# Kernel tuning notes

Hardware: AMD Instinct MI355X
Metric: run time of the kernel (lower is better)

## Reference

```python
import jax, jax.numpy as jnp
import numpy as np

C = 64           # channels
CPG = 8          # channel_per_group
G = C // CPG     # offset groups = 8
K = 27           # 3x3x3 taps
N, D, H, W = 2, 8, 56, 56


def conv3d(x, w, b=None):
    y = jax.lax.conv_general_dilated(
        x, w, window_strides=(1, 1, 1), padding=[(1, 1)] * 3,
        dimension_numbers=('NCDHW', 'OIDHW', 'NCDHW'))
    if b is not None:
        y = y + b.reshape(1, -1, 1, 1, 1)
    return y


def deform_conv3d(x, off, w, groups):
    # x: [N,C,D,H,W]; off: [N, G*3*27, D,H,W]; w: [O,C,3,3,3]
    n, cin, d, h, wd = x.shape
    cpg = cin // groups
    p = d * h * wd
    off = off.reshape(n, groups, K, 3, d, h, wd)
    # kernel tap displacements in (kd,kh,kw) order, each in {-1,0,1}
    r = jnp.arange(3, dtype=x.dtype) - 1.0
    taps = jnp.stack(jnp.meshgrid(r, r, r, indexing='ij'), axis=-1).reshape(K, 3)
    gd = jnp.arange(d, dtype=x.dtype)[:, None, None]
    gh = jnp.arange(h, dtype=x.dtype)[None, :, None]
    gw = jnp.arange(wd, dtype=x.dtype)[None, None, :]
    # sampling positions [N,G,K,D,H,W]
    pd = gd + taps[:, 0][:, None, None, None] + off[:, :, :, 0]
    ph = gh + taps[:, 1][:, None, None, None] + off[:, :, :, 1]
    pw = gw + taps[:, 2][:, None, None, None] + off[:, :, :, 2]
    d0 = jnp.floor(pd); h0 = jnp.floor(ph); w0 = jnp.floor(pw)
    fd, fh, fw = pd - d0, ph - h0, pw - w0
    d0 = d0.astype(jnp.int32); h0 = h0.astype(jnp.int32); w0 = w0.astype(jnp.int32)
    xflat = x.reshape(n, groups, cpg, p)[:, :, None]  # [N,G,1,Cpg,P]
    acc = jnp.zeros((n, groups, K, cpg, p), x.dtype)
    for cd in (0, 1):
        for ch in (0, 1):
            for cw in (0, 1):
                idd, idh, idw = d0 + cd, h0 + ch, w0 + cw
                wgt = ((fd if cd else 1.0 - fd)
                       * (fh if ch else 1.0 - fh)
                       * (fw if cw else 1.0 - fw))
                valid = ((idd >= 0) & (idd < d) & (idh >= 0) & (idh < h)
                         & (idw >= 0) & (idw < wd)).astype(x.dtype)
                lin = ((jnp.clip(idd, 0, d - 1) * h + jnp.clip(idh, 0, h - 1)) * wd
                       + jnp.clip(idw, 0, wd - 1))
                g = jnp.take_along_axis(xflat, lin.reshape(n, groups, K, 1, p), axis=-1)
                acc = acc + g * (wgt * valid).reshape(n, groups, K, 1, p)
    # [N,G,K,Cpg,P] -> [N,K,C,P]
    vals = acc.transpose(0, 2, 1, 3, 4).reshape(n, K, cin, p)
    out = jnp.einsum('oik,nkip->nop', w.reshape(w.shape[0], cin, K), vals)
    return out.reshape(n, -1, d, h, wd)


def batchnorm(x, gamma, beta, eps=1e-5):
    m = x.mean((0, 2, 3, 4), keepdims=True)
    v = x.var((0, 2, 3, 4), keepdims=True)
    return (gamma.reshape(1, -1, 1, 1, 1) * (x - m) * jax.lax.rsqrt(v + eps)
            + beta.reshape(1, -1, 1, 1, 1))


def setup_inputs() -> dict:
    key = jax.random.key(0)
    ks = jax.random.split(key, 4)
    fan = C * K
    x = jax.random.normal(ks[0], (N, C, D, H, W), jnp.float32)
    w_off = jax.random.normal(ks[1], (G * 3 * K, C, 3, 3, 3), jnp.float32) * 0.01
    b_off = jnp.zeros((G * 3 * K,), jnp.float32)
    w1 = jax.random.normal(ks[2], (C, C, 3, 3, 3), jnp.float32) / np.sqrt(fan).astype(np.float32)
    w2 = jax.random.normal(ks[3], (C, C, 3, 3, 3), jnp.float32) / np.sqrt(fan).astype(np.float32)
    return dict(x=x, w_off=w_off, b_off=b_off, w1=w1,
                gamma1=jnp.ones((C,), jnp.float32), beta1=jnp.zeros((C,), jnp.float32),
                w2=w2, b2=jnp.zeros((C,), jnp.float32),
                gamma2=jnp.ones((C,), jnp.float32), beta2=jnp.zeros((C,), jnp.float32))


def reference(x, w_off, b_off, w1, gamma1, beta1, w2, b2, gamma2, beta2):
    residual = x
    off = conv3d(x, w_off, b_off)
    out = deform_conv3d(x, off, w1, G)
    out = jax.nn.relu(batchnorm(out, gamma1, beta1))
    out = conv3d(out, w2, b2)
    out = batchnorm(out, gamma2, beta2) + residual
    return jax.nn.relu(out)
```

## Files before the change

kernel.cpp:

```cpp
#include <hip/hip_runtime.h>
#include <hip/hip_bf16.h>

#define N_ 2
#define C_ 64
#define D_ 8
#define H_ 56
#define W_ 56
#define HW_ (H_*W_)
#define P_ (D_*HW_)
#define G_ 8
#define CPG_ 8
#define K_ 27
#define CO_OFF_ 648
#define MP_ 768
#define KK_ 1728
#define KB_ (KK_*2)

typedef __attribute__((ext_vector_type(8))) short shortx8;
typedef __attribute__((ext_vector_type(4))) float floatx4;
#define AS1 __attribute__((address_space(1)))
#define AS3 __attribute__((address_space(3)))

__device__ inline float b2f(unsigned short u) {
    union { unsigned u; float f; } x; x.u = ((unsigned)u) << 16; return x.f;
}
__device__ inline unsigned short f2b(float f) {
    union { float f; unsigned u; } x; x.f = f;
    unsigned r = (x.u + 0x7fffu + ((x.u >> 16) & 1u)) >> 16;
    return (unsigned short)r;
}
__device__ inline float lof(unsigned u) { union { unsigned u; float f; } x; x.u = u << 16; return x.f; }
__device__ inline float hif(unsigned u) { union { unsigned u; float f; } x; x.u = u & 0xffff0000u; return x.f; }
__device__ inline unsigned cvt_pk_bf16(float a, float b) {
    unsigned r;
    asm("v_cvt_pk_bf16_f32 %0, %1, %2" : "=v"(r) : "v"(a), "v"(b));
    return r;
}


__global__ __launch_bounds__(256) void transpose_xt_kernel(
    const float* __restrict__ x, unsigned short* __restrict__ xt)
{
    __shared__ unsigned short tile[64][65];
    int b  = blockIdx.x;
    int n  = b / (P_/64);
    int p0 = (b % (P_/64))*64;
    int tid = threadIdx.x;
    int j  = tid & 63;
    int c0 = (tid >> 6)*16;
    for (int r = 0; r < 16; ++r)
        tile[c0 + r][j] = f2b(x[((size_t)n*C_ + c0 + r)*P_ + p0 + j]);
    __syncthreads();
    unsigned* dst = (unsigned*)(xt + ((size_t)n*P_ + p0)*C_);
    #pragma unroll
    for (int it = 0; it < 8; ++it) {
        int wi  = it*256 + tid;
        int row = wi >> 5;
        int c   = (wi & 31)*2;
        unsigned lo = tile[c][row], hi = tile[c+1][row];
        dst[(size_t)row*32 + (wi & 31)] = lo | (hi << 16);
    }
}

__global__ __launch_bounds__(256) void permA1k_kernel(
    const float* __restrict__ w, unsigned short* __restrict__ A)
{
    int i = blockIdx.x*256 + threadIdx.x;
    if (i >= MP_*KK_) return;
    int m = i / KK_, r = i % KK_;
    int kk = r / 64, ci = r % 64;
    A[i] = (m < CO_OFF_) ? f2b(w[((size_t)m*C_ + ci)*K_ + kk]) : (unsigned short)0;
}

__global__ __launch_bounds__(256) void perm_w_kernel(
    const float* __restrict__ w, unsigned short* __restrict__ At)
{
    int tid = blockIdx.x*256 + threadIdx.x;
    if (tid >= C_*KK_) return;
    int o  = tid / KK_;
    int r  = tid % KK_;
    int k  = r / 64, i = r % 64;
    At[tid] = f2b(w[((size_t)o*C_ + i)*K_ + k]);
}

__global__ __launch_bounds__(256, 2) void conv_off_fused(
    const unsigned short* __restrict__ A,
    const unsigned short* __restrict__ xt,
    const float* __restrict__ bias,
    unsigned short* __restrict__ off2)
{
    __shared__ __align__(16) short SH[35840];
    int tid = threadIdx.x;
    int w = tid >> 6, lane = tid & 63;
    int lm = lane & 15, lq = lane >> 4;

    if (blockIdx.x < 2*490) {
        short* As0 = SH;
        short* Bs  = SH + 2*16*512;
        int n   = blockIdx.x / 490;
        int bid = blockIdx.x % 490;
        int mt = bid / 98, nt = bid % 98;
        int m0 = mt*128, p0 = nt*256;

        const unsigned short* xtn = xt + (size_t)n*P_*C_;
        unsigned short* out2 = off2 + (size_t)n*216*P_*3;

        const char* Ab0 = (const char*)A + (size_t)(m0 + w*32 + lm)*KB_ + lq*16;
        const char* Ab1 = Ab0 + (size_t)16*KB_;

        int oct = lane & 7;
        int prj[8], dj[8], hj[8], wj[8];
        #pragma unroll
        for (int j = 0; j < 8; ++j) {
            int prow = j*32 + w*8 + (lane >> 3);
            prj[j] = prow;
            int p = p0 + prow;
            dj[j] = p / HW_;
            int hw2 = p % HW_;
            hj[j] = hw2 / W_;
            wj[j] = hw2 % W_;
        }

        auto stageA = [&](int kt, int buf) {
            __builtin_amdgcn_global_load_lds((const AS1 unsigned*)(Ab0 + kt*128),      (AS3 unsigned*)(As0 + buf*8192 + (w*2)*512),     16, 0, 0);
            __builtin_amdgcn_global_load_lds((const AS1 unsigned*)(Ab1 + kt*128),      (AS3 unsigned*)(As0 + buf*8192 + (w*2+1)*512),   16, 0, 0);
            __builtin_amdgcn_global_load_lds((const AS1 unsigned*)(Ab0 + kt*128 + 64), (AS3 unsigned*)(As0 + buf*8192 + (8+w*2)*512),   16, 0, 0);
            __builtin_amdgcn_global_load_lds((const AS1 unsigned*)(Ab1 + kt*128 + 64), (AS3 unsigned*)(As0 + buf*8192 + (8+w*2+1)*512), 16, 0, 0);
        };
        auto loadB = [&](int kt, uint4* B) {
            int kd = kt/9 - 1, kh = (kt/3)%3 - 1, kw = kt%3 - 1;
            int delta = kd*HW_ + kh*W_ + kw;
            #pragma unroll
            for (int j = 0; j < 8; ++j) {
                bool v = ((unsigned)(dj[j]+kd) < (unsigned)D_) &&
                         ((unsigned)(hj[j]+kh) < (unsigned)H_) &&
                         ((unsigned)(wj[j]+kw) < (unsigned)W_);
                uint4 val = {0u,0u,0u,0u};
                if (v) val = *(const uint4*)(xtn + (size_t)(p0 + prj[j] + delta)*C_ + oct*8);
                B[j] = val;
            }
        };

        int mh = w >> 1, nh = w & 1;
        floatx4 acc[4][8];
        #pragma unroll
        for (int i = 0; i < 4; ++i)
            #pragma unroll
            for (int j = 0; j < 8; ++j)
                acc[i][j] = (floatx4){0.f, 0.f, 0.f, 0.f};

        uint4 Bcur[8], Bnext[8];
        #pragma unroll
        for (int j = 0; j < 8; ++j) Bnext[j] = (uint4){0u,0u,0u,0u};
        stageA(0, 0);
        loadB(0, Bcur);

        for (int kt = 0; kt < 27; ++kt) {
            int buf = kt & 1;
            __syncthreads();
            #pragma unroll
            for (int j = 0; j < 8; ++j) {
                int chunk = (oct>>2)*16 + (prj[j]>>4);
                *(uint4*)&Bs[chunk*512 + ((oct&3)*16 + ((prj[j]&15) ^ oct))*8] = Bcur[j];
            }
            __syncthreads();
            if (kt < 26) { stageA(kt+1, buf^1); loadB(kt+1, Bnext); }
            #pragma unroll
            for (int ks = 0; ks < 2; ++ks) {
                int swzB = (lq*16 + (lm ^ (ks*4 + lq)))*8;
                shortx8 a[4];
                #pragma unroll
                for (int i = 0; i < 4; ++i) a[i] = *(const shortx8*)&As0[buf*8192 + (ks*8 + 4*mh + i)*512 + lane*8];
                #pragma unroll
                for (int j = 0; j < 8; ++j) {
                    shortx8 b = *(const shortx8*)&Bs[(ks*16 + 8*nh + j)*512 + swzB];
                    #pragma unroll
                    for (int i = 0; i < 4; ++i)
                        acc[i][j] = __builtin_amdgcn_mfma_f32_16x16x32_bf16(a[i], b, acc[i][j], 0, 0, 0);
                }
            }
            #pragma unroll
            for (int j = 0; j < 8; ++j) Bcur[j] = Bnext[j];
        }

        #pragma unroll
        for (int i = 0; i < 4; ++i) {
            int cob = m0 + (4*mh+i)*16 + lq*4;
            #pragma unroll
            for (int r = 0; r < 4; ++r) {
                int co = cob + r;
                float bv = bias[co];
                int row2 = co / 3, comp = co % 3;
                size_t base = (size_t)row2*P_*3 + comp;
                #pragma unroll
                for (int j = 0; j < 8; ++j) {
                    int col = p0 + (8*nh+j)*16 + lm;
                    out2[base + (size_t)col*3] = f2b(acc[i][j][r] + bv);
                }
            }
        }
    } else {
        short* As = SH;
        short* Bs = SH + 54*512;
        int t  = blockIdx.x - 2*490;
        int n  = t / 196;
        int p0 = (t % 196)*128;

        const unsigned short* xtn = xt + (size_t)n*P_*C_;
        unsigned short* out2 = off2 + (size_t)n*216*P_*3;

        const char* Abase = (const char*)A + (size_t)(640 + lm)*KB_ + lq*16;
        for (int ch = w; ch < 54; ch += 4)
            __builtin_amdgcn_global_load_lds((const AS1 unsigned*)(Abase + ch*64),
                                             (AS3 unsigned*)(As + ch*512), 16, 0, 0);

        int oct = lane & 7;
        int prj[4], dj[4], hj[4], wj[4];
        #pragma unroll
        for (int j = 0; j < 4; ++j) {
            int prow = j*32 + w*8 + (lane >> 3);
            prj[j] = prow;
            int p = p0 + prow;
            dj[j] = p / HW_;
            int hw2 = p % HW_;
            hj[j] = hw2 / W_;
            wj[j] = hw2 % W_;
        }
        auto loadB = [&](int kt, uint4* B) {
            int kd = kt/9 - 1, kh = (kt/3)%3 - 1, kw = kt%3 - 1;
            int delta = kd*HW_ + kh*W_ + kw;
            #pragma unroll
            for (int j = 0; j < 4; ++j) {
                bool v = ((unsigned)(dj[j]+kd) < (unsigned)D_) &&
                         ((unsigned)(hj[j]+kh) < (unsigned)H_) &&
                         ((unsigned)(wj[j]+kw) < (unsigned)W_);
                uint4 val = {0u,0u,0u,0u};
                if (v) val = *(const uint4*)(xtn + (size_t)(p0 + prj[j] + delta)*C_ + oct*8);
                B[j] = val;
            }
        };

        floatx4 acc[2];
        acc[0] = (floatx4){0.f,0.f,0.f,0.f};
        acc[1] = (floatx4){0.f,0.f,0.f,0.f};

        uint4 Bcur[4], Bnext[4];
        #pragma unroll
        for (int j = 0; j < 4; ++j) Bnext[j] = (uint4){0u,0u,0u,0u};
        loadB(0, Bcur);

        for (int kt = 0; kt < 27; ++kt) {
            __syncthreads();
            #pragma unroll
            for (int j = 0; j < 4; ++j) {
                int chunk = (oct>>2)*8 + (prj[j]>>4);
                *(uint4*)&Bs[chunk*512 + ((oct&3)*16 + ((prj[j]&15) ^ oct))*8] = Bcur[j];
            }
            __syncthreads();
            if (kt < 26) loadB(kt+1, Bnext);
            #pragma unroll
            for (int ks = 0; ks < 2; ++ks) {
                int swzB = (lq*16 + (lm ^ (ks*4 + lq)))*8;
                shortx8 a = *(const shortx8*)&As[(kt*2 + ks)*512 + lane*8];
                #pragma unroll
                for (int j = 0; j < 2; ++j) {
                    shortx8 b = *(const shortx8*)&Bs[(ks*8 + w*2 + j)*512 + swzB];
                    acc[j] = __builtin_amdgcn_mfma_f32_16x16x32_bf16(a, b, acc[j], 0, 0, 0);
                }
            }
            #pragma unroll
            for (int j = 0; j < 4; ++j) Bcur[j] = Bnext[j];
        }

        #pragma unroll
        for (int j = 0; j < 2; ++j) {
            #pragma unroll
            for (int r = 0; r < 4; ++r) {
                int co = 640 + lq*4 + r;
                if (co < CO_OFF_) {
                    int col = p0 + w*32 + j*16 + lm;
                    out2[((size_t)(co/3)*P_ + col)*3 + (co%3)] = f2b(acc[j][r] + bias[co]);
                }
            }
        }
    }
}

__global__ __launch_bounds__(256) void deform_fused(
    const unsigned short* __restrict__ xt,
    const unsigned short* __restrict__ off2,
    const unsigned short* __restrict__ A,
    unsigned short* __restrict__ y1t)
{
    __shared__ __align__(16) short SH[12288];
    int tid = threadIdx.x;
    int w = tid >> 6, lane = tid & 63;
    int n  = blockIdx.x / (P_/32);
    int p0 = (blockIdx.x % (P_/32))*32;
    int lm = lane & 15, lq = lane >> 4;

    const unsigned short* offn = off2 + (size_t)n*216*P_*3;
    const uint4* xg0 = (const uint4*)(xt + (size_t)n*P_*C_);

    const char* Ab = (const char*)A + (size_t)(w*16 + lm)*KB_ + lq*16;

    int g = lane & 7;
    int prow = tid >> 3;
    int p = p0 + prow;
    int dd = p / HW_;
    int hw2 = p % HW_;
    int hh = hw2 / W_;
    int ww = hw2 % W_;
    int bchunk = (g>>2)*2 + (prow>>4);
    int boffs  = ((g&3)*16 + ((prow&15) ^ g))*8;

    auto stageA = [&](int kt, int buf) {
        __builtin_amdgcn_global_load_lds((const AS1 unsigned*)(Ab + kt*128),      (AS3 unsigned*)(SH + buf*4096 + w*512),     16, 0, 0);
        __builtin_amdgcn_global_load_lds((const AS1 unsigned*)(Ab + kt*128 + 64), (AS3 unsigned*)(SH + buf*4096 + (4+w)*512), 16, 0, 0);
    };
    auto loadOff = [&](int kt, float* o) {
        size_t idx = ((size_t)(g*K_ + kt)*P_ + p)*3;
        o[0] = b2f(offn[idx]);
        o[1] = b2f(offn[idx + 1]);
        o[2] = b2f(offn[idx + 2]);
    };
    auto issueCorners = [&](int kt, float* o, uint4* V, float* Wt) {
        int kd = kt/9 - 1, kh = (kt/3)%3 - 1, kw = kt%3 - 1;
        float pd = (float)(dd + kd) + o[0];
        float ph = (float)(hh + kh) + o[1];
        float pw = (float)(ww + kw) + o[2];
        float fd0 = floorf(pd), fh0 = floorf(ph), fw0 = floorf(pw);
        int d0 = (int)fd0, h0 = (int)fh0, w0i = (int)fw0;
        float fd = pd - fd0, fh = ph - fh0, fw = pw - fw0;
        int dc0 = min(max(d0, 0), D_-1),   dc1 = min(max(d0+1, 0), D_-1);
        int hc0 = min(max(h0, 0), H_-1),   hc1 = min(max(h0+1, 0), H_-1);
        int wc0 = min(max(w0i, 0), W_-1),  wc1 = min(max(w0i+1, 0), W_-1);
        float wd0 = ((unsigned)d0      < (unsigned)D_) ? 1.f - fd : 0.f;
        float wd1 = ((unsigned)(d0+1)  < (unsigned)D_) ? fd       : 0.f;
        float wh0 = ((unsigned)h0      < (unsigned)H_) ? 1.f - fh : 0.f;
        float wh1 = ((unsigned)(h0+1)  < (unsigned)H_) ? fh       : 0.f;
        float ww0 = ((unsigned)w0i     < (unsigned)W_) ? 1.f - fw : 0.f;
        float ww1 = ((unsigned)(w0i+1) < (unsigned)W_) ? fw       : 0.f;
        int rb00 = (dc0*H_ + hc0)*W_, rb01 = (dc0*H_ + hc1)*W_;
        int rb10 = (dc1*H_ + hc0)*W_, rb11 = (dc1*H_ + hc1)*W_;
        float wdh00 = wd0*wh0, wdh01 = wd0*wh1, wdh10 = wd1*wh0, wdh11 = wd1*wh1;
        V[0] = xg0[(size_t)(rb00+wc0)*8 + g];  Wt[0] = wdh00*ww0;
        V[1] = xg0[(size_t)(rb00+wc1)*8 + g];  Wt[1] = wdh00*ww1;
        V[2] = xg0[(size_t)(rb01+wc0)*8 + g];  Wt[2] = wdh01*ww0;
        V[3] = xg0[(size_t)(rb01+wc1)*8 + g];  Wt[3] = wdh01*ww1;
        V[4] = xg0[(size_t)(rb10+wc0)*8 + g];  Wt[4] = wdh10*ww0;
        V[5] = xg0[(size_t)(rb10+wc1)*8 + g];  Wt[5] = wdh10*ww1;
        V[6] = xg0[(size_t)(rb11+wc0)*8 + g];  Wt[6] = wdh11*ww0;
        V[7] = xg0[(size_t)(rb11+wc1)*8 + g];  Wt[7] = wdh11*ww1;
    };
    auto reduceCorners = [&](uint4* V, float* Wt, uint4& o4) {
        float res[CPG_];
        #pragma unroll
        for (int c = 0; c < CPG_; ++c) res[c] = 0.f;
        #pragma unroll
        for (int c = 0; c < 8; ++c) {
            uint4 v4 = V[c];
            float wgt = Wt[c];
            res[0] = fmaf(wgt, lof(v4.x), res[0]);
            res[1] = fmaf(wgt, hif(v4.x), res[1]);
            res[2] = fmaf(wgt, lof(v4.y), res[2]);
            res[3] = fmaf(wgt, hif(v4.y), res[3]);
            res[4] = fmaf(wgt, lof(v4.z), res[4]);
            res[5] = fmaf(wgt, hif(v4.z), res[5]);
            res[6] = fmaf(wgt, lof(v4.w), res[6]);
            res[7] = fmaf(wgt, hif(v4.w), res[7]);
        }
        o4.x = cvt_pk_bf16(res[0], res[1]);
        o4.y = cvt_pk_bf16(res[2], res[3]);
        o4.z = cvt_pk_bf16(res[4], res[5]);
        o4.w = cvt_pk_bf16(res[6], res[7]);
    };

    int mh = w >> 1, nh = w & 1;
    floatx4 acc[2];
    acc[0] = (floatx4){0.f,0.f,0.f,0.f};
    acc[1] = (floatx4){0.f,0.f,0.f,0.f};

    float offA[3], offB[3], offT[3];
    uint4 Vv[8]; float Wt[8];
    uint4 o4cur;

    stageA(0, 0);
    loadOff(0, offA);
    loadOff(1, offB);
    issueCorners(0, offA, Vv, Wt);
    reduceCorners(Vv, Wt, o4cur);
    *(uint4*)&SH[8192 + bchunk*512 + boffs] = o4cur;

    for (int kt = 0; kt < 27; ++kt) {
        int buf = kt & 1;
        __syncthreads();
        if (kt < 26) {
            stageA(kt+1, buf^1);
            if (kt < 25) loadOff(kt+2, offT);
            issueCorners(kt+1, offB, Vv, Wt);
        }
        #pragma unroll
        for (int ks = 0; ks < 2; ++ks) {
            int swzB = (lq*16 + (lm ^ (ks*4 + lq)))*8;
            shortx8 b = *(const shortx8*)&SH[8192 + buf*2048 + (ks*2 + nh)*512 + swzB];
            #pragma unroll
            for (int i = 0; i < 2; ++i) {
                shortx8 a = *(const shortx8*)&SH[buf*4096 + (ks*4 + 2*mh+i)*512 + lane*8];
                acc[i] = __builtin_amdgcn_mfma_f32_16x16x32_bf16(a, b, acc[i], 0, 0, 0);
            }
        }
        if (kt < 26) {
            reduceCorners(Vv, Wt, o4cur);
            *(uint4*)&SH[8192 + (buf^1)*2048 + bchunk*512 + boffs] = o4cur;
            offB[0] = offT[0]; offB[1] = offT[1]; offB[2] = offT[2];
        }
    }

    __syncthreads();
    #pragma unroll
    for (int i = 0; i < 2; ++i) {
        int ob = mh*32 + i*16 + lq*4;
        int pc = nh*16 + lm;
        #pragma unroll
        for (int rr = 0; rr < 4; ++rr)
            SH[pc*72 + ob + rr] = (short)f2b(acc[i][rr]);
    }
    __syncthreads();
    {
        int row = tid >> 3, seg = tid & 7;
        uint4 v = *(const uint4*)&SH[row*72 + seg*8];
        *(uint4*)(y1t + ((size_t)n*P_ + p0 + row)*C_ + seg*8) = v;
    }
}

__global__ __launch_bounds__(256) void conv2_fused(
    const unsigned short* __restrict__ y1t,
    const float* __restrict__ st1,
    const unsigned short* __restrict__ A,
    const float* __restrict__ bias,
    unsigned short* __restrict__ y2,
    float* __restrict__ part2)
{
    __shared__ __align__(16) short As[4][4096];
    __shared__ float sc[64], sf[64];
    __shared__ float SP[4][64], SQ[4][64];
    int tid = threadIdx.x;
    if (tid < 64) sc[tid] = st1[tid];
    else if (tid < 128) sf[tid-64] = st1[tid];
    int w = tid >> 6, lane = tid & 63;
    int n  = blockIdx.x / (P_/64);
    int p0 = (blockIdx.x % (P_/64))*64;
    int lm = lane & 15, lq = lane >> 4;

    const unsigned short* y1n = y1t + (size_t)n*P_*C_;
    unsigned short* y2n = y2 + (size_t)n*C_*P_;
    const char* Ab = (const char*)A + (size_t)(w*16 + lm)*KB_ + lq*16;

    int p = p0 + w*16 + lm;
    int dd = p / HW_, hw2 = p % HW_;
    int hh = hw2 / W_, ww = hw2 % W_;

    auto stageA = [&](int kt) {
        int buf = kt & 3;
        __builtin_amdgcn_global_load_lds((const AS1 unsigned*)(Ab + kt*128),      (AS3 unsigned*)(&As[buf][w*512]),     16, 0, 0);
        __builtin_amdgcn_global_load_lds((const AS1 unsigned*)(Ab + kt*128 + 64), (AS3 unsigned*)(&As[buf][(4+w)*512]), 16, 0, 0);
    };
    auto issueV = [&](int kt, uint4* V, int& M) {
        int kd = kt/9 - 1, kh = (kt/3)%3 - 1, kw = kt%3 - 1;
        int delta = kd*HW_ + kh*W_ + kw;
        bool v = ((unsigned)(dd+kd) < (unsigned)D_) &&
                 ((unsigned)(hh+kh) < (unsigned)H_) &&
                 ((unsigned)(ww+kw) < (unsigned)W_);
        M = v ? 1 : 0;
        #pragma unroll
        for (int ks = 0; ks < 2; ++ks) {
            uint4 val = {0u,0u,0u,0u};
            if (v) val = *(const uint4*)(y1n + (size_t)(p + delta)*C_ + (ks*4 + lq)*8);
            V[ks] = val;
        }
    };
    auto reduceT = [&](uint4 V, int ks, int M) -> shortx8 {
        uint4 o4 = {0u,0u,0u,0u};
        if (M) {
            int cb = (ks*4 + lq)*8;
            float r0 = fmaxf(lof(V.x)*sc[cb+0] + sf[cb+0], 0.f);
            float r1 = fmaxf(hif(V.x)*sc[cb+1] + sf[cb+1], 0.f);
            float r2 = fmaxf(lof(V.y)*sc[cb+2] + sf[cb+2], 0.f);
            float r3 = fmaxf(hif(V.y)*sc[cb+3] + sf[cb+3], 0.f);
            float r4 = fmaxf(lof(V.z)*sc[cb+4] + sf[cb+4], 0.f);
            float r5 = fmaxf(hif(V.z)*sc[cb+5] + sf[cb+5], 0.f);
            float r6 = fmaxf(lof(V.w)*sc[cb+6] + sf[cb+6], 0.f);
            float r7 = fmaxf(hif(V.w)*sc[cb+7] + sf[cb+7], 0.f);
            o4.x = cvt_pk_bf16(r0, r1);
            o4.y = cvt_pk_bf16(r2, r3);
            o4.z = cvt_pk_bf16(r4, r5);
            o4.w = cvt_pk_bf16(r6, r7);
        }
        return *(shortx8*)&o4;
    };

    floatx4 acc[4];
    #pragma unroll
    for (int i = 0; i < 4; ++i) acc[i] = (floatx4){0.f,0.f,0.f,0.f};

    auto mfmaTap = [&](int kt, shortx8 b0, shortx8 b1) {
        int buf = kt & 3;
        #pragma unroll
        for (int i = 0; i < 4; ++i) {
            shortx8 a = *(const shortx8*)&As[buf][(0*4 + i)*512 + lane*8];
            acc[i] = __builtin_amdgcn_mfma_f32_16x16x32_bf16(a, b0, acc[i], 0, 0, 0);
        }
        #pragma unroll
        for (int i = 0; i < 4; ++i) {
            shortx8 a = *(const shortx8*)&As[buf][(1*4 + i)*512 + lane*8];
            acc[i] = __builtin_amdgcn_mfma_f32_16x16x32_bf16(a, b1, acc[i], 0, 0, 0);
        }
    };

    uint4 VA[2], VB[2];
    int MA, MB;
    stageA(0); stageA(1);
    issueV(0, VA, MA);
    issueV(1, VB, MB);

    for (int kt = 0; kt < 26; kt += 2) {
        __syncthreads();
        stageA(kt+2);
        if (kt+3 <= 26) stageA(kt+3);
        {
            shortx8 b0 = reduceT(VA[0], 0, MA);
            shortx8 b1 = reduceT(VA[1], 1, MA);
            issueV(kt+2, VA, MA);
            mfmaTap(kt, b0, b1);
        }
        {
            shortx8 b0 = reduceT(VB[0], 0, MB);
            shortx8 b1 = reduceT(VB[1], 1, MB);
            if (kt+3 <= 26) issueV(kt+3, VB, MB);
            mfmaTap(kt+1, b0, b1);
        }
    }
    __syncthreads();
    {
        shortx8 b0 = reduceT(VA[0], 0, MA);
        shortx8 b1 = reduceT(VA[1], 1, MA);
        mfmaTap(26, b0, b1);
    }

    #pragma unroll
    for (int i = 0; i < 4; ++i) {
        #pragma unroll
        for (int r = 0; r < 4; ++r) {
            int co = i*16 + lq*4 + r;
            float v = acc[i][r] + bias[co];
            y2n[(size_t)co*P_ + p] = f2b(v);
            float s = v, q = v*v;
            #pragma unroll
            for (int m = 1; m < 16; m <<= 1) {
                s += __shfl_xor(s, m);
                q += __shfl_xor(q, m);
            }
            if (lm == 0) { SP[w][co] = s; SQ[w][co] = q; }
        }
    }
    __syncthreads();
    if (tid < 64) {
        float S = SP[0][tid] + SP[1][tid] + SP[2][tid] + SP[3][tid];
        float Q = SQ[0][tid] + SQ[1][tid] + SQ[2][tid] + SQ[3][tid];
        part2[(size_t)blockIdx.x*128 + tid]      = S;
        part2[(size_t)blockIdx.x*128 + 64 + tid] = Q;
    }
}

__global__ __launch_bounds__(256) void stats_partial_kernel(
    const unsigned short* __restrict__ y1t, float* __restrict__ part)
{
    int b = blockIdx.x, tid = threadIdx.x;
    int c = tid & 63, sub = tid >> 6;
    float s = 0.f, q = 0.f;
    for (int rr = 0; rr < 128; ++rr) {
        int row = b*512 + sub*128 + rr;
        float v = b2f(y1t[(size_t)row*C_ + c]);
        s += v;
        q = fmaf(v, v, q);
    }
    __shared__ float ss[256], qq[256];
    ss[tid] = s; qq[tid] = q;
    __syncthreads();
    if (tid < 64) {
        float S = ss[tid] + ss[64+tid] + ss[128+tid] + ss[192+tid];
        float Q = qq[tid] + qq[64+tid] + qq[128+tid] + qq[192+tid];
        part[b*128 + tid]      = S;
        part[b*128 + 64 + tid] = Q;
    }
}

__global__ void stats_final_kernel(
    const float* __restrict__ part,
    const float* __restrict__ gamma, const float* __restrict__ beta,
    float* __restrict__ st1)
{
    int c = threadIdx.x;
    float S = 0.f, Q = 0.f;
    for (int b = 0; b < 98; ++b) {
        S += part[b*128 + c];
        Q += part[b*128 + 64 + c];
    }
    const float inv = 1.f / (float)(N_*P_);
    float m = S * inv;
    float var = Q * inv - m*m;
    float scale = rsqrtf(var + 1e-5f) * gamma[c];
    st1[c]      = scale;
    st1[64 + c] = beta[c] - m*scale;
}

__global__ __launch_bounds__(256) void bn2_final_kernel(
    const float* __restrict__ part2,
    const float* __restrict__ gamma, const float* __restrict__ beta,
    float* __restrict__ st2)
{
    int tid = threadIdx.x;
    int c = tid & 63, seg = tid >> 6;
    float S = 0.f, Q = 0.f;
    for (int b = seg*196; b < seg*196 + 196; ++b) {
        S += part2[(size_t)b*128 + c];
        Q += part2[(size_t)b*128 + 64 + c];
    }
    __shared__ float ss[256], qq[256];
    ss[tid] = S; qq[tid] = Q;
    __syncthreads();
    if (tid < 64) {
        float St = ss[tid] + ss[64+tid] + ss[128+tid] + ss[192+tid];
        float Qt = qq[tid] + qq[64+tid] + qq[128+tid] + qq[192+tid];
        const float inv = 1.f / (float)(N_*P_);
        float m = St * inv;
        float var = Qt * inv - m*m;
        float scale = rsqrtf(var + 1e-5f) * gamma[tid];
        st2[tid]      = scale;
        st2[64 + tid] = beta[tid] - m*scale;
    }
}

__global__ __launch_bounds__(256) void bn_add_relu_kernel(
    const unsigned short* __restrict__ y2, const float* __restrict__ x,
    const float* __restrict__ st2, float* __restrict__ out)
{
    size_t i4 = ((size_t)blockIdx.x*256 + threadIdx.x)*4;
    int c = (int)((i4 / P_) % C_);
    float scale = st2[c], shift = st2[64 + c];
    uint2 yv = *(const uint2*)(y2 + i4);
    float4 xv = *(const float4*)(x + i4);
    float4 o;
    o.x = fmaxf(fmaf(lof(yv.x), scale, shift) + xv.x, 0.f);
    o.y = fmaxf(fmaf(hif(yv.x), scale, shift) + xv.y, 0.f);
    o.z = fmaxf(fmaf(lof(yv.y), scale, shift) + xv.z, 0.f);
    o.w = fmaxf(fmaf(hif(yv.y), scale, shift) + xv.w, 0.f);
    *(float4*)(out + i4) = o;
}

extern "C" void kernel_launch(void* const* d_in, const int* in_sizes, int n_in,
                              void* d_out, int out_size, void* d_ws, size_t ws_size,
                              hipStream_t stream) {
    const float* x     = (const float*)d_in[0];
    const float* w_off = (const float*)d_in[1];
    const float* b_off = (const float*)d_in[2];
    const float* w1    = (const float*)d_in[3];
    const float* g1    = (const float*)d_in[4];
    const float* be1   = (const float*)d_in[5];
    const float* w2    = (const float*)d_in[6];
    const float* b2    = (const float*)d_in[7];
    const float* g2    = (const float*)d_in[8];
    const float* be2   = (const float*)d_in[9];
    float* out = (float*)d_out;

    float* st1  = (float*)d_ws;
    float* st2  = st1 + 128;
    float* part = st2 + 128;
    unsigned short* off2 = (unsigned short*)(part + 98*128);
    unsigned short* xt  = off2 + (size_t)N_*216*P_*3;
    unsigned short* y1t = xt  + (size_t)N_*P_*C_;
    unsigned short* y2  = y1t + (size_t)N_*P_*C_;
    unsigned short* A1k = y2  + (size_t)N_*C_*P_;
    unsigned short* A1t = A1k + (size_t)MP_*KK_;
    unsigned short* A2t = A1t + (size_t)C_*KK_;
    float* part2 = (float*)off2;

    transpose_xt_kernel<<<N_*(P_/64), 256, 0, stream>>>(x, xt);
    permA1k_kernel<<<(MP_*KK_+255)/256, 256, 0, stream>>>(w_off, A1k);
    perm_w_kernel<<<(C_*KK_+255)/256, 256, 0, stream>>>(w1, A1t);
    perm_w_kernel<<<(C_*KK_+255)/256, 256, 0, stream>>>(w2, A2t);

    conv_off_fused<<<2*490 + 2*196, 256, 0, stream>>>(A1k, xt, b_off, off2);

    deform_fused<<<N_*(P_/32), 256, 0, stream>>>(xt, off2, A1t, y1t);

    stats_partial_kernel<<<98, 256, 0, stream>>>(y1t, part);
    stats_final_kernel<<<1, 64, 0, stream>>>(part, g1, be1, st1);

    conv2_fused<<<N_*(P_/64), 256, 0, stream>>>(y1t, st1, A2t, b2, y2, part2);

    bn2_final_kernel<<<1, 256, 0, stream>>>(part2, g2, be2, st2);
    bn_add_relu_kernel<<<(N_*C_*P_)/1024, 256, 0, stream>>>(y2, x, st2, out);
}
```

Baseline: 467.0 us.

## Merge prep kernels, fuse BN1 stats into deform, widen conv2 tiles

Merges the four input and weight preparation kernels into one launch. Computes the BN1 partial sums inside the deform kernel epilogue from the staged LDS tile, which removes a separate pass that re-read y1t. Doubles the conv2 pixel tile to 128 per block so each A-tile in LDS feeds two MFMA column groups, at the cost of more registers and fewer blocks. The final stats kernels are resized to match the new partial counts.

```diff
diff --git a/kernel.cpp b/kernel.cpp
--- a/kernel.cpp
+++ b/kernel.cpp
@@ -38,49 +38,49 @@
 }
 
 
-__global__ __launch_bounds__(256) void transpose_xt_kernel(
-    const float* __restrict__ x, unsigned short* __restrict__ xt)
+__global__ __launch_bounds__(256) void prep_kernel(
+    const float* __restrict__ x,      unsigned short* __restrict__ xt,
+    const float* __restrict__ w_off,  unsigned short* __restrict__ A1k,
+    const float* __restrict__ w1,     unsigned short* __restrict__ A1t,
+    const float* __restrict__ w2,     unsigned short* __restrict__ A2t)
 {
     __shared__ unsigned short tile[64][65];
-    int b  = blockIdx.x;
-    int n  = b / (P_/64);
-    int p0 = (b % (P_/64))*64;
+    int b   = blockIdx.x;
     int tid = threadIdx.x;
-    int j  = tid & 63;
-    int c0 = (tid >> 6)*16;
-    for (int r = 0; r < 16; ++r)
-        tile[c0 + r][j] = f2b(x[((size_t)n*C_ + c0 + r)*P_ + p0 + j]);
-    __syncthreads();
-    unsigned* dst = (unsigned*)(xt + ((size_t)n*P_ + p0)*C_);
-    #pragma unroll
-    for (int it = 0; it < 8; ++it) {
-        int wi  = it*256 + tid;
-        int row = wi >> 5;
-        int c   = (wi & 31)*2;
-        unsigned lo = tile[c][row], hi = tile[c+1][row];
-        dst[(size_t)row*32 + (wi & 31)] = lo | (hi << 16);
-    }
-}
-
-__global__ __launch_bounds__(256) void permA1k_kernel(
-    const float* __restrict__ w, unsigned short* __restrict__ A)
-{
-    int i = blockIdx.x*256 + threadIdx.x;
-    if (i >= MP_*KK_) return;
-    int m = i / KK_, r = i % KK_;
-    int kk = r / 64, ci = r % 64;
-    A[i] = (m < CO_OFF_) ? f2b(w[((size_t)m*C_ + ci)*K_ + kk]) : (unsigned short)0;
-}
-
-__global__ __launch_bounds__(256) void perm_w_kernel(
-    const float* __restrict__ w, unsigned short* __restrict__ At)
-{
-    int tid = blockIdx.x*256 + threadIdx.x;
-    if (tid >= C_*KK_) return;
-    int o  = tid / KK_;
-    int r  = tid % KK_;
-    int k  = r / 64, i = r % 64;
-    At[tid] = f2b(w[((size_t)o*C_ + i)*K_ + k]);
+
+    if (b < 784) {
+        int n  = b / (P_/64);
+        int p0 = (b % (P_/64))*64;
+        int j  = tid & 63;
+        int c0 = (tid >> 6)*16;
+        for (int r = 0; r < 16; ++r)
+            tile[c0 + r][j] = f2b(x[((size_t)n*C_ + c0 + r)*P_ + p0 + j]);
+        __syncthreads();
+        unsigned* dst = (unsigned*)(xt + ((size_t)n*P_ + p0)*C_);
+        #pragma unroll
+        for (int it = 0; it < 8; ++it) {
+            int wi  = it*256 + tid;
+            int row = wi >> 5;
+            int c   = (wi & 31)*2;
+            unsigned lo = tile[c][row], hi = tile[c+1][row];
+            dst[(size_t)row*32 + (wi & 31)] = lo | (hi << 16);
+        }
+    } else if (b < 784 + 5184) {
+        int i = (b - 784)*256 + tid;
+        int m = i / KK_, r = i % KK_;
+        int kk = r / 64, ci = r % 64;
+        A1k[i] = (m < CO_OFF_) ? f2b(w_off[((size_t)m*C_ + ci)*K_ + kk]) : (unsigned short)0;
+    } else if (b < 784 + 5184 + 432) {
+        int i = (b - 784 - 5184)*256 + tid;
+        int o = i / KK_, r = i % KK_;
+        int k = r / 64, ii = r % 64;
+        A1t[i] = f2b(w1[((size_t)o*C_ + ii)*K_ + k]);
+    } else {
+        int i = (b - 784 - 5184 - 432)*256 + tid;
+        int o = i / KK_, r = i % KK_;
+        int k = r / 64, ii = r % 64;
+        A2t[i] = f2b(w2[((size_t)o*C_ + ii)*K_ + k]);
+    }
 }
 
 __global__ __launch_bounds__(256, 2) void conv_off_fused(
@@ -290,7 +290,8 @@
     const unsigned short* __restrict__ xt,
     const unsigned short* __restrict__ off2,
     const unsigned short* __restrict__ A,
-    unsigned short* __restrict__ y1t)
+    unsigned short* __restrict__ y1t,
+    float* __restrict__ bn1p)
 {
     __shared__ __align__(16) short SH[12288];
     int tid = threadIdx.x;
@@ -432,6 +433,27 @@
         uint4 v = *(const uint4*)&SH[row*72 + seg*8];
         *(uint4*)(y1t + ((size_t)n*P_ + p0 + row)*C_ + seg*8) = v;
     }
+    {
+        float* FS = (float*)(SH + 2560);
+        float* FQ = FS + 256;
+        int o = tid & 63, qt = tid >> 6;
+        float s = 0.f, q = 0.f;
+        #pragma unroll
+        for (int pp = 0; pp < 8; ++pp) {
+            float v = b2f((unsigned short)SH[(qt*8 + pp)*72 + o]);
+            s += v;
+            q = fmaf(v, v, q);
+        }
+        FS[qt*64 + o] = s;
+        FQ[qt*64 + o] = q;
+        __syncthreads();
+        if (tid < 64) {
+            float S = FS[tid] + FS[64+tid] + FS[128+tid] + FS[192+tid];
+            float Q = FQ[tid] + FQ[64+tid] + FQ[128+tid] + FQ[192+tid];
+            bn1p[(size_t)blockIdx.x*128 + tid]      = S;
+            bn1p[(size_t)blockIdx.x*128 + 64 + tid] = Q;
+        }
+    }
 }
 
 __global__ __launch_bounds__(256) void conv2_fused(
@@ -449,35 +471,44 @@
     if (tid < 64) sc[tid] = st1[tid];
     else if (tid < 128) sf[tid-64] = st1[tid];
     int w = tid >> 6, lane = tid & 63;
-    int n  = blockIdx.x / (P_/64);
-    int p0 = (blockIdx.x % (P_/64))*64;
+    int n  = blockIdx.x / (P_/128);
+    int p0 = (blockIdx.x % (P_/128))*128;
     int lm = lane & 15, lq = lane >> 4;
 
     const unsigned short* y1n = y1t + (size_t)n*P_*C_;
     unsigned short* y2n = y2 + (size_t)n*C_*P_;
     const char* Ab = (const char*)A + (size_t)(w*16 + lm)*KB_ + lq*16;
 
-    int p = p0 + w*16 + lm;
-    int dd = p / HW_, hw2 = p % HW_;
-    int hh = hw2 / W_, ww = hw2 % W_;
+    int pj[2], dd[2], hh[2], ww[2];
+    #pragma unroll
+    for (int j = 0; j < 2; ++j) {
+        pj[j] = p0 + j*64 + w*16 + lm;
+        dd[j] = pj[j] / HW_;
+        int hw2 = pj[j] % HW_;
+        hh[j] = hw2 / W_;
+        ww[j] = hw2 % W_;
+    }
 
     auto stageA = [&](int kt) {
         int buf = kt & 3;
         __builtin_amdgcn_global_load_lds((const AS1 unsigned*)(Ab + kt*128),      (AS3 unsigned*)(&As[buf][w*512]),     16, 0, 0);
         __builtin_amdgcn_global_load_lds((const AS1 unsigned*)(Ab + kt*128 + 64), (AS3 unsigned*)(&As[buf][(4+w)*512]), 16, 0, 0);
     };
-    auto issueV = [&](int kt, uint4* V, int& M) {
+    auto issueV = [&](int kt, uint4 (*V)[2], int* M) {
         int kd = kt/9 - 1, kh = (kt/3)%3 - 1, kw = kt%3 - 1;
         int delta = kd*HW_ + kh*W_ + kw;
-        bool v = ((unsigned)(dd+kd) < (unsigned)D_) &&
-                 ((unsigned)(hh+kh) < (unsigned)H_) &&
-                 ((unsigned)(ww+kw) < (unsigned)W_);
-        M = v ? 1 : 0;
-        #pragma unroll
-        for (int ks = 0; ks < 2; ++ks) {
-            uint4 val = {0u,0u,0u,0u};
-            if (v) val = *(const uint4*)(y1n + (size_t)(p + delta)*C_ + (ks*4 + lq)*8);
-            V[ks] = val;
+        #pragma unroll
+        for (int j = 0; j < 2; ++j) {
+            bool v = ((unsigned)(dd[j]+kd) < (unsigned)D_) &&
+                     ((unsigned)(hh[j]+kh) < (unsigned)H_) &&
+                     ((unsigned)(ww[j]+kw) < (unsigned)W_);
+            M[j] = v ? 1 : 0;
+            #pragma unroll
+            for (int ks = 0; ks < 2; ++ks) {
+                uint4 val = {0u,0u,0u,0u};
+                if (v) val = *(const uint4*)(y1n + (size_t)(pj[j] + delta)*C_ + (ks*4 + lq)*8);
+                V[j][ks] = val;
+            }
         }
     };
     auto reduceT = [&](uint4 V, int ks, int M) -> shortx8 {
@@ -500,26 +531,34 @@
         return *(shortx8*)&o4;
     };
 
-    floatx4 acc[4];
+    floatx4 acc[4][2];
     #pragma unroll
-    for (int i = 0; i < 4; ++i) acc[i] = (floatx4){0.f,0.f,0.f,0.f};
-
-    auto mfmaTap = [&](int kt, shortx8 b0, shortx8 b1) {
+    for (int i = 0; i < 4; ++i)
+        #pragma unroll
+        for (int j = 0; j < 2; ++j)
+            acc[i][j] = (floatx4){0.f,0.f,0.f,0.f};
+
+    auto mfmaTap = [&](int kt, uint4 (*V)[2], const int* M) {
         int buf = kt & 3;
         #pragma unroll
-        for (int i = 0; i < 4; ++i) {
-            shortx8 a = *(const shortx8*)&As[buf][(0*4 + i)*512 + lane*8];
-            acc[i] = __builtin_amdgcn_mfma_f32_16x16x32_bf16(a, b0, acc[i], 0, 0, 0);
-        }
-        #pragma unroll
-        for (int i = 0; i < 4; ++i) {
-            shortx8 a = *(const shortx8*)&As[buf][(1*4 + i)*512 + lane*8];
-            acc[i] = __builtin_amdgcn_mfma_f32_16x16x32_bf16(a, b1, acc[i], 0, 0, 0);
+        for (int j = 0; j < 2; ++j) {
+            shortx8 b0 = reduceT(V[j][0], 0, M[j]);
+            shortx8 b1 = reduceT(V[j][1], 1, M[j]);
+            #pragma unroll
+            for (int i = 0; i < 4; ++i) {
+                shortx8 a = *(const shortx8*)&As[buf][(0*4 + i)*512 + lane*8];
+                acc[i][j] = __builtin_amdgcn_mfma_f32_16x16x32_bf16(a, b0, acc[i][j], 0, 0, 0);
+            }
+            #pragma unroll
+            for (int i = 0; i < 4; ++i) {
+                shortx8 a = *(const shortx8*)&As[buf][(1*4 + i)*512 + lane*8];
+                acc[i][j] = __builtin_amdgcn_mfma_f32_16x16x32_bf16(a, b1, acc[i][j], 0, 0, 0);
+            }
         }
     };
 
-    uint4 VA[2], VB[2];
-    int MA, MB;
+    uint4 VA[2][2], VB[2][2];
+    int MA[2], MB[2];
     stageA(0); stageA(1);
     issueV(0, VA, MA);
     issueV(1, VB, MB);
@@ -529,33 +568,36 @@
         stageA(kt+2);
         if (kt+3 <= 26) stageA(kt+3);
         {
-            shortx8 b0 = reduceT(VA[0], 0, MA);
-            shortx8 b1 = reduceT(VA[1], 1, MA);
+            uint4 Vc[2][2];
+            #pragma unroll
+            for (int j = 0; j < 2; ++j) { Vc[j][0] = VA[j][0]; Vc[j][1] = VA[j][1]; }
+            int Mc[2] = {MA[0], MA[1]};
             issueV(kt+2, VA, MA);
-            mfmaTap(kt, b0, b1);
+            mfmaTap(kt, Vc, Mc);
         }
         {
-            shortx8 b0 = reduceT(VB[0], 0, MB);
-            shortx8 b1 = reduceT(VB[1], 1, MB);
+            uint4 Vc[2][2];
+            #pragma unroll
+            for (int j = 0; j < 2; ++j) { Vc[j][0] = VB[j][0]; Vc[j][1] = VB[j][1]; }
+            int Mc[2] = {MB[0], MB[1]};
             if (kt+3 <= 26) issueV(kt+3, VB, MB);
-            mfmaTap(kt+1, b0, b1);
+            mfmaTap(kt+1, Vc, Mc);
         }
     }
     __syncthreads();
-    {
-        shortx8 b0 = reduceT(VA[0], 0, MA);
-        shortx8 b1 = reduceT(VA[1], 1, MA);
-        mfmaTap(26, b0, b1);
-    }
+    mfmaTap(26, VA, MA);
 
     #pragma unroll
     for (int i = 0; i < 4; ++i) {
         #pragma unroll
         for (int r = 0; r < 4; ++r) {
             int co = i*16 + lq*4 + r;
-            float v = acc[i][r] + bias[co];
-            y2n[(size_t)co*P_ + p] = f2b(v);
-            float s = v, q = v*v;
+            float v0 = acc[i][0][r] + bias[co];
+            float v1 = acc[i][1][r] + bias[co];
+            y2n[(size_t)co*P_ + pj[0]] = f2b(v0);
+            y2n[(size_t)co*P_ + pj[1]] = f2b(v1);
+            float s = v0 + v1;
+            float q = v0*v0 + v1*v1;
             #pragma unroll
             for (int m = 1; m < 16; m <<= 1) {
                 s += __shfl_xor(s, m);
@@ -573,46 +615,31 @@
     }
 }
 
-__global__ __launch_bounds__(256) void stats_partial_kernel(
-    const unsigned short* __restrict__ y1t, float* __restrict__ part)
-{
-    int b = blockIdx.x, tid = threadIdx.x;
-    int c = tid & 63, sub = tid >> 6;
-    float s = 0.f, q = 0.f;
-    for (int rr = 0; rr < 128; ++rr) {
-        int row = b*512 + sub*128 + rr;
-        float v = b2f(y1t[(size_t)row*C_ + c]);
-        s += v;
-        q = fmaf(v, v, q);
-    }
-    __shared__ float ss[256], qq[256];
-    ss[tid] = s; qq[tid] = q;
-    __syncthreads();
-    if (tid < 64) {
-        float S = ss[tid] + ss[64+tid] + ss[128+tid] + ss[192+tid];
-        float Q = qq[tid] + qq[64+tid] + qq[128+tid] + qq[192+tid];
-        part[b*128 + tid]      = S;
-        part[b*128 + 64 + tid] = Q;
-    }
-}
-
-__global__ void stats_final_kernel(
+__global__ __launch_bounds__(256) void stats_final_kernel(
     const float* __restrict__ part,
     const float* __restrict__ gamma, const float* __restrict__ beta,
     float* __restrict__ st1)
 {
-    int c = threadIdx.x;
+    int tid = threadIdx.x;
+    int c = tid & 63, seg = tid >> 6;
     float S = 0.f, Q = 0.f;
-    for (int b = 0; b < 98; ++b) {
-        S += part[b*128 + c];
-        Q += part[b*128 + 64 + c];
-    }
-    const float inv = 1.f / (float)(N_*P_);
-    float m = S * inv;
-    float var = Q * inv - m*m;
-    float scale = rsqrtf(var + 1e-5f) * gamma[c];
-    st1[c]      = scale;
-    st1[64 + c] = beta[c] - m*scale;
+    for (int b = seg*392; b < seg*392 + 392; ++b) {
+        S += part[(size_t)b*128 + c];
+        Q += part[(size_t)b*128 + 64 + c];
+    }
+    __shared__ float ss[256], qq[256];
+    ss[tid] = S; qq[tid] = Q;
+    __syncthreads();
+    if (tid < 64) {
+        float St = ss[tid] + ss[64+tid] + ss[128+tid] + ss[192+tid];
+        float Qt = qq[tid] + qq[64+tid] + qq[128+tid] + qq[192+tid];
+        const float inv = 1.f / (float)(N_*P_);
+        float m = St * inv;
+        float var = Qt * inv - m*m;
+        float scale = rsqrtf(var + 1e-5f) * gamma[tid];
+        st1[tid]      = scale;
+        st1[64 + tid] = beta[tid] - m*scale;
+    }
 }
 
 __global__ __launch_bounds__(256) void bn2_final_kernel(
@@ -623,7 +650,7 @@
     int tid = threadIdx.x;
     int c = tid & 63, seg = tid >> 6;
     float S = 0.f, Q = 0.f;
-    for (int b = seg*196; b < seg*196 + 196; ++b) {
+    for (int b = seg*98; b < seg*98 + 98; ++b) {
         S += part2[(size_t)b*128 + c];
         Q += part2[(size_t)b*128 + 64 + c];
     }
@@ -676,8 +703,8 @@
 
     float* st1  = (float*)d_ws;
     float* st2  = st1 + 128;
-    float* part = st2 + 128;
-    unsigned short* off2 = (unsigned short*)(part + 98*128);
+    float* bn1p = st2 + 128;
+    unsigned short* off2 = (unsigned short*)(bn1p + 1568*128);
     unsigned short* xt  = off2 + (size_t)N_*216*P_*3;
     unsigned short* y1t = xt  + (size_t)N_*P_*C_;
     unsigned short* y2  = y1t + (size_t)N_*P_*C_;
@@ -686,19 +713,16 @@
     unsigned short* A2t = A1t + (size_t)C_*KK_;
     float* part2 = (float*)off2;
 
-    transpose_xt_kernel<<<N_*(P_/64), 256, 0, stream>>>(x, xt);
-    permA1k_kernel<<<(MP_*KK_+255)/256, 256, 0, stream>>>(w_off, A1k);
-    perm_w_kernel<<<(C_*KK_+255)/256, 256, 0, stream>>>(w1, A1t);
-    perm_w_kernel<<<(C_*KK_+255)/256, 256, 0, stream>>>(w2, A2t);
+    prep_kernel<<<784 + 5184 + 432 + 432, 256, 0, stream>>>(
+        x, xt, w_off, A1k, w1, A1t, w2, A2t);
 
     conv_off_fused<<<2*490 + 2*196, 256, 0, stream>>>(A1k, xt, b_off, off2);
 
-    deform_fused<<<N_*(P_/32), 256, 0, stream>>>(xt, off2, A1t, y1t);
-
-    stats_partial_kernel<<<98, 256, 0, stream>>>(y1t, part);
-    stats_final_kernel<<<1, 64, 0, stream>>>(part, g1, be1, st1);
-
-    conv2_fused<<<N_*(P_/64), 256, 0, stream>>>(y1t, st1, A2t, b2, y2, part2);
+    deform_fused<<<N_*(P_/32), 256, 0, stream>>>(xt, off2, A1t, y1t, bn1p);
+
+    stats_final_kernel<<<1, 256, 0, stream>>>(bn1p, g1, be1, st1);
+
+    conv2_fused<<<N_*(P_/128), 256, 0, stream>>>(y1t, st1, A2t, b2, y2, part2);
 
     bn2_final_kernel<<<1, 256, 0, stream>>>(part2, g2, be2, st2);
     bn_add_relu_kernel<<<(N_*C_*P_)/1024, 256, 0, stream>>>(y2, x, st2, out);
```

Result: faster. 452.7 us, median of 2 (-3.1%).
